# Kernel tuning notes

Hardware: AMD Instinct MI355X
Metric: run time of the kernel (lower is better)

Reference implementation:

```python
import jax, jax.numpy as jnp
import numpy as np

B, D, N = 2, 128, 100000  # batch, cubic grid edge, active voxels


def _conv(x, w):
    # valid 3D conv, NDHWC activations, DHWIO weights
    return jax.lax.conv_general_dilated(
        x, w, window_strides=(1, 1, 1), padding='VALID',
        dimension_numbers=('NDHWC', 'DHWIO', 'NDHWC'))


def setup_inputs() -> dict:
    key = jax.random.key(0)
    k = jax.random.split(key, 7)
    bidx = jax.random.randint(k[0], (N, 1), 0, B, dtype=jnp.int32)
    sp = jax.random.randint(k[1], (N, 3), 0, D, dtype=jnp.int32)
    coords = jnp.concatenate([bidx, sp], axis=1)          # [N,4] (b,z,y,x)
    voxels = jax.random.normal(k[2], (N, 3), jnp.float32)  # [N,3]
    W1 = jax.random.normal(k[3], (2, 2, 2, 3, 9), jnp.float32) * 0.2   # spconv1
    W2 = jax.random.normal(k[4], (3, 3, 3, 9, 5), jnp.float32) * 0.1   # spconv2
    W3 = jax.random.normal(k[5], (3, 3, 3, 5, 3), jnp.float32) * 0.1   # normal_conv3d
    b3 = jax.random.normal(k[6], (3,), jnp.float32) * 0.1
    return {'coords': coords, 'voxels': voxels, 'W1': W1, 'W2': W2, 'W3': W3, 'b3': b3}


def reference(coords, voxels, W1, W2, W3, b3):
    # scatter sparse voxels into a dense grid [B,D,D,D,3]
    dense = jnp.zeros((B, D, D, D, voxels.shape[-1]), voxels.dtype)
    dense = dense.at[coords[:, 0], coords[:, 1], coords[:, 2], coords[:, 3]].add(voxels)
    # SparseConv3d (stride=1, pad=0) == valid dense conv on the densified tensor
    x = _conv(dense, W1)      # [B,127,127,127,9]
    x = _conv(x, W2)          # [B,125,125,125,5]  (== ScatterDense of sparse out)
    x = _conv(x, W3) + b3     # [B,123,123,123,3]
    return jax.nn.relu(x)
```

## Files before the change

### kernel.cpp

```cpp
#include <hip/hip_runtime.h>
#include <hip/hip_bf16.h>

#define DGRID 128
#define E1 127
#define E2 125
#define E3 123

typedef __attribute__((ext_vector_type(8))) short short8;
typedef __attribute__((ext_vector_type(4))) float f32x4;
typedef __attribute__((ext_vector_type(4))) unsigned int u32x4;

static __device__ __forceinline__ unsigned short f2bf(float f) {
    union { __hip_bfloat16 h; unsigned short u; } cv;
    cv.h = __float2bfloat16(f);
    return cv.u;
}

static __device__ __forceinline__ int r3off(int row, int x) {
    return row * 384 + ((x * 16) ^ ((row & 7) << 4));
}

__global__ __launch_bounds__(256) void zero_k(float4* __restrict__ p, int n4) {
    int i = blockIdx.x * 256 + threadIdx.x;
    if (i < n4) p[i] = make_float4(0.f, 0.f, 0.f, 0.f);
}

__global__ __launch_bounds__(256) void scatter_k(const int* __restrict__ coords,
                                                 const float* __restrict__ voxels,
                                                 float* __restrict__ dense, int N) {
    int i = blockIdx.x * blockDim.x + threadIdx.x;
    if (i >= N * 3) return;
    int n = i / 3, c = i - n * 3;
    int b = coords[n * 4 + 0];
    int z = coords[n * 4 + 1];
    int y = coords[n * 4 + 2];
    int x = coords[n * 4 + 3];
    int idx = (((b * DGRID + z) * DGRID + y) * DGRID + x) * 4 + c;
    atomicAdd(&dense[idx], voxels[n * 3 + c]);
}

__global__ __launch_bounds__(256) void wcomp_k(const float* __restrict__ W1f,
                                               const float* __restrict__ W2f,
                                               float* __restrict__ W12) {
    for (int e = threadIdx.x; e < 960; e += 256) {
        const int tap = e / 15, r = e % 15;
        const int ci = r / 5, co = r % 5;
        const int KZ = tap >> 4, KY = (tap >> 2) & 3, KX = tap & 3;
        float acc = 0.f;
#pragma unroll
        for (int k1z = 0; k1z < 2; ++k1z) {
            const int k2z = KZ - k1z;
            if (k2z < 0 || k2z > 2) continue;
#pragma unroll
            for (int k1y = 0; k1y < 2; ++k1y) {
                const int k2y = KY - k1y;
                if (k2y < 0 || k2y > 2) continue;
#pragma unroll
                for (int k1x = 0; k1x < 2; ++k1x) {
                    const int k2x = KX - k1x;
                    if (k2x < 0 || k2x > 2) continue;
                    const float* w1 = W1f + ((k1z * 2 + k1y) * 2 + k1x) * 27 + ci * 9;
                    const float* w2 = W2f + ((k2z * 3 + k2y) * 3 + k2x) * 45 + co;
#pragma unroll
                    for (int m = 0; m < 9; ++m) acc += w1[m] * w2[m * 5];
                }
            }
        }
        W12[tap * 15 + r] = acc;
    }
}

__global__ __launch_bounds__(256, 4) void conv12_k(const float* __restrict__ dense,
                                                   const float* __restrict__ W12,
                                                   short* __restrict__ x2s) {
    __shared__ __align__(16) char sDD[19360];

    const int tid = threadIdx.x;
    int blk = blockIdx.x;
    const int xt  = blk & 7;  blk >>= 3;
    const int tyt = blk & 15; blk >>= 4;
    const int tzt = blk & 15; blk >>= 4;
    const int b   = blk;
    const int z0 = tzt * 8, y0 = tyt * 8, x0 = xt * 16;

    const int lane = tid & 63;
    const int col  = lane & 15;
    const int q4   = lane >> 4;
    const int wv   = tid >> 6;

    short8 B12[8];
#pragma unroll
    for (int t = 0; t < 8; ++t) {
#pragma unroll
        for (int j = 0; j < 8; ++j) {
            const int tap = 8 * t + 2 * q4 + (j >> 2);
            const int ci  = j & 3;
            float v = (ci < 3 && col < 5) ? W12[tap * 15 + ci * 5 + col] : 0.f;
            B12[t][j] = (short)f2bf(v);
        }
    }

    int offt[8];
#pragma unroll
    for (int t = 0; t < 8; ++t) {
        const int T0 = 8 * t + 2 * q4;
        const int kz = T0 >> 4, ky = (T0 >> 2) & 3, kx0 = T0 & 3;
        offt[t] = (kz * 11 + ky) * 160 + kx0 * 8;
    }

#pragma unroll 1
    for (int p = tid; p < 2299; p += 256) {
        const int xp = p % 19; int t2 = p / 19;
        const int yp = t2 % 11; const int zp = t2 / 11;
        const int gz = min(z0 + zp, DGRID - 1);
        const int gy = min(y0 + yp, DGRID - 1);
        const int gx = min(x0 + xp, DGRID - 1);
        const float4 v = *(const float4*)(dense +
            (size_t)(((b * DGRID + gz) * DGRID + gy) * DGRID + gx) * 4);
        const unsigned lo = (unsigned)f2bf(v.x) | ((unsigned)f2bf(v.y) << 16);
        const unsigned hi = (unsigned)f2bf(v.z) | ((unsigned)f2bf(v.w) << 16);
        *(uint2*)(sDD + (zp * 11 + yp) * 160 + xp * 8) = make_uint2(lo, hi);
    }
    __syncthreads();

#pragma unroll 1
    for (int gi = 0; gi < 16; ++gi) {
        const int g = wv * 16 + gi;
        const int zp = g >> 3, yp = g & 7;
        const int oz = z0 + zp, oy = y0 + yp;
        if (oz >= E2 || oy >= E2) continue;
        const int baseg = (zp * 11 + yp) * 160 + col * 8;
        f32x4 acc = {0.f, 0.f, 0.f, 0.f};
#pragma unroll
        for (int t = 0; t < 8; ++t) {
            const char* p = sDD + baseg + offt[t];
            const uint2 ra = *(const uint2*)(p);
            const uint2 rb = *(const uint2*)(p + 8);
            union { u32x4 u; short8 s; } av;
            av.u[0] = ra.x; av.u[1] = ra.y; av.u[2] = rb.x; av.u[3] = rb.y;
            acc = __builtin_amdgcn_mfma_f32_16x16x32_bf16(av.s, B12[t], acc, 0, 0, 0);
        }
        if (col < 8) {
#pragma unroll
            for (int jj = 0; jj < 4; ++jj) {
                const int ox = x0 + q4 * 4 + jj;
                if (ox < E2)
                    x2s[(size_t)(((b * E2 + oz) * E2 + oy) * E2 + ox) * 8 + col] =
                        (short)f2bf(acc[jj]);
            }
        }
    }
}

__global__ __launch_bounds__(256, 4) void conv3_k(const short* __restrict__ x2s,
                                                  const float* __restrict__ W3f,
                                                  const float* __restrict__ b3f,
                                                  float* __restrict__ out) {
    __shared__ __align__(16) char sX2[38400];

    const int tid = threadIdx.x;
    int blk = blockIdx.x;
    const int xt  = blk & 7;  blk >>= 3;
    const int tyt = blk & 15; blk >>= 4;
    const int tzt = blk & 15; blk >>= 4;
    const int b   = blk;
    const int z0 = tzt * 8, y0 = tyt * 8, x0 = xt * 16;

#pragma unroll 1
    for (int p = tid; p < 1800; p += 256) {
        const int xp = p % 18; int t2 = p / 18;
        const int yp = t2 % 10; const int zp = t2 / 10;
        const int iz = min(z0 + zp, E2 - 1);
        const int iy = min(y0 + yp, E2 - 1);
        const int ix = min(x0 + xp, E2 - 1);
        const short8 rec = *(const short8*)(x2s + (size_t)(((b * E2 + iz) * E2 + iy) * E2 + ix) * 8);
        *(short8*)(sX2 + r3off(zp * 10 + yp, xp)) = rec;
    }

    const int lane = tid & 63;
    const int col  = lane & 15;
    const int q4   = lane >> 4;
    short8 B3[7];
#pragma unroll
    for (int t = 0; t < 7; ++t) {
        const int tap = 4 * t + q4;
#pragma unroll
        for (int j = 0; j < 8; ++j) {
            float v = 0.f;
            if (tap < 27 && j < 5 && col < 3) v = W3f[(tap * 5 + j) * 3 + col];
            B3[t][j] = (short)f2bf(v);
        }
    }
    const float bias = (col < 3) ? b3f[col] : 0.f;
    __syncthreads();

    const int wv = tid >> 6;
#pragma unroll 1
    for (int gi = 0; gi < 16; ++gi) {
        const int g = wv * 16 + gi;
        const int zp = g >> 3, yp = g & 7;
        const int oz = z0 + zp, oy = y0 + yp;
        if (oz >= E3 || oy >= E3) continue;
        f32x4 acc = {0.f, 0.f, 0.f, 0.f};
#pragma unroll
        for (int t = 0; t < 7; ++t) {
            const int tap = (4 * t + q4 > 26) ? 26 : 4 * t + q4;
            const int kz = tap / 9, ky = (tap / 3) % 3, kx = tap % 3;
            const int row = (zp + kz) * 10 + (yp + ky);
            const int xi = (lane & 15) + kx;
            const short8 a = *(const short8*)(sX2 + r3off(row, xi));
            acc = __builtin_amdgcn_mfma_f32_16x16x32_bf16(a, B3[t], acc, 0, 0, 0);
        }
        if (col < 3) {
#pragma unroll
            for (int jj = 0; jj < 4; ++jj) {
                const int ox = x0 + q4 * 4 + jj;
                if (ox < E3)
                    out[(size_t)(((b * E3 + oz) * E3 + oy) * E3 + ox) * 3 + col] =
                        fmaxf(acc[jj] + bias, 0.f);
            }
        }
    }
}

extern "C" void kernel_launch(void* const* d_in, const int* in_sizes, int n_in,
                              void* d_out, int out_size, void* d_ws, size_t ws_size,
                              hipStream_t stream) {
    const int*   coords = (const int*)d_in[0];
    const float* voxels = (const float*)d_in[1];
    const float* W1     = (const float*)d_in[2];
    const float* W2     = (const float*)d_in[3];
    const float* W3     = (const float*)d_in[4];
    const float* b3     = (const float*)d_in[5];
    float* out = (float*)d_out;

    const int N = in_sizes[0] / 4;

    char* ws = (char*)d_ws;
    const size_t dense_elems = (size_t)2 * DGRID * DGRID * DGRID * 4;
    const size_t dense_bytes = dense_elems * sizeof(float);
    const size_t x2_bytes    = (size_t)2 * E2 * E2 * E2 * 8 * sizeof(short);
    float* dense = (float*)ws;
    short* x2s   = (short*)(ws + dense_bytes);
    float* W12   = (float*)(ws + dense_bytes + x2_bytes);

    const int n4 = (int)(dense_elems / 4);
    zero_k<<<(n4 + 255) / 256, 256, 0, stream>>>((float4*)dense, n4);

    scatter_k<<<(N * 3 + 255) / 256, 256, 0, stream>>>(coords, voxels, dense, N);

    wcomp_k<<<1, 256, 0, stream>>>(W1, W2, W12);

    const int nblk12 = 2 * 16 * 16 * 8;
    conv12_k<<<nblk12, 256, 0, stream>>>(dense, W12, x2s);

    const int nblk3 = 2 * 16 * 16 * 8;
    conv3_k<<<nblk3, 256, 0, stream>>>(x2s, W3, b3, out);
}
```

Baseline: 229.8 us.

## Batch rows per wave and duplicate odd-shifted LDS tile for aligned 16B loads

In conv12_k, the dense tile is stored twice in LDS, a second copy shifted by one voxel, so each MFMA A-operand becomes a single aligned 16-byte load instead of two 8-byte loads. Both conv kernels now process several output rows per wave with independent accumulators. This exposes more MFMA ILP and removes per-row index math. conv3_k drops the XOR swizzle for a padded 336-byte row stride. The costs are doubled LDS in conv12 (possibly lower occupancy), more registers, and possible bank conflicts from the changed layout.

```diff
diff --git a/kernel.cpp b/kernel.cpp
--- a/kernel.cpp
+++ b/kernel.cpp
@@ -8,16 +8,11 @@
 
 typedef __attribute__((ext_vector_type(8))) short short8;
 typedef __attribute__((ext_vector_type(4))) float f32x4;
-typedef __attribute__((ext_vector_type(4))) unsigned int u32x4;
 
 static __device__ __forceinline__ unsigned short f2bf(float f) {
     union { __hip_bfloat16 h; unsigned short u; } cv;
     cv.h = __float2bfloat16(f);
     return cv.u;
-}
-
-static __device__ __forceinline__ int r3off(int row, int x) {
-    return row * 384 + ((x * 16) ^ ((row & 7) << 4));
 }
 
 __global__ __launch_bounds__(256) void zero_k(float4* __restrict__ p, int n4) {
@@ -73,7 +68,7 @@
 __global__ __launch_bounds__(256, 4) void conv12_k(const float* __restrict__ dense,
                                                    const float* __restrict__ W12,
                                                    short* __restrict__ x2s) {
-    __shared__ __align__(16) char sDD[19360];
+    __shared__ __align__(16) char sDD[38720];
 
     const int tid = threadIdx.x;
     int blk = blockIdx.x;
@@ -100,12 +95,13 @@
         }
     }
 
-    int offt[8];
+    int ofs[8];
 #pragma unroll
     for (int t = 0; t < 8; ++t) {
         const int T0 = 8 * t + 2 * q4;
         const int kz = T0 >> 4, ky = (T0 >> 2) & 3, kx0 = T0 & 3;
-        offt[t] = (kz * 11 + ky) * 160 + kx0 * 8;
+        const int s = col + kx0;
+        ofs[t] = (kz * 11 + ky) * 160 + ((s & 1) ? (19360 + (s - 1) * 8) : (s * 8));
     }
 
 #pragma unroll 1
@@ -119,34 +115,39 @@
             (size_t)(((b * DGRID + gz) * DGRID + gy) * DGRID + gx) * 4);
         const unsigned lo = (unsigned)f2bf(v.x) | ((unsigned)f2bf(v.y) << 16);
         const unsigned hi = (unsigned)f2bf(v.z) | ((unsigned)f2bf(v.w) << 16);
-        *(uint2*)(sDD + (zp * 11 + yp) * 160 + xp * 8) = make_uint2(lo, hi);
+        const int off = (zp * 11 + yp) * 160 + xp * 8;
+        *(uint2*)(sDD + off) = make_uint2(lo, hi);
+        if (xp > 0) *(uint2*)(sDD + 19360 + off - 8) = make_uint2(lo, hi);
     }
     __syncthreads();
 
 #pragma unroll 1
-    for (int gi = 0; gi < 16; ++gi) {
-        const int g = wv * 16 + gi;
-        const int zp = g >> 3, yp = g & 7;
-        const int oz = z0 + zp, oy = y0 + yp;
-        if (oz >= E2 || oy >= E2) continue;
-        const int baseg = (zp * 11 + yp) * 160 + col * 8;
-        f32x4 acc = {0.f, 0.f, 0.f, 0.f};
+    for (int batch = 0; batch < 4; ++batch) {
+        const int zp = wv * 2 + (batch >> 1);
+        const int yb = (batch & 1) * 4;
+        const int rowb = (zp * 11 + yb) * 160;
+        f32x4 acc[4];
+#pragma unroll
+        for (int i = 0; i < 4; ++i) acc[i] = (f32x4){0.f, 0.f, 0.f, 0.f};
 #pragma unroll
         for (int t = 0; t < 8; ++t) {
-            const char* p = sDD + baseg + offt[t];
-            const uint2 ra = *(const uint2*)(p);
-            const uint2 rb = *(const uint2*)(p + 8);
-            union { u32x4 u; short8 s; } av;
-            av.u[0] = ra.x; av.u[1] = ra.y; av.u[2] = rb.x; av.u[3] = rb.y;
-            acc = __builtin_amdgcn_mfma_f32_16x16x32_bf16(av.s, B12[t], acc, 0, 0, 0);
-        }
-        if (col < 8) {
-#pragma unroll
-            for (int jj = 0; jj < 4; ++jj) {
-                const int ox = x0 + q4 * 4 + jj;
-                if (ox < E2)
-                    x2s[(size_t)(((b * E2 + oz) * E2 + oy) * E2 + ox) * 8 + col] =
-                        (short)f2bf(acc[jj]);
+            const char* pa = sDD + rowb + ofs[t];
+#pragma unroll
+            for (int i = 0; i < 4; ++i) {
+                const short8 a = *(const short8*)(pa + i * 160);
+                acc[i] = __builtin_amdgcn_mfma_f32_16x16x32_bf16(a, B12[t], acc[i], 0, 0, 0);
+            }
+        }
+        const int oz = z0 + zp;
+#pragma unroll
+        for (int i = 0; i < 4; ++i) {
+            const int oy = y0 + yb + i;
+            if (oz < E2 && oy < E2 && col < 8) {
+                short* op = x2s + (size_t)(((b * E2 + oz) * E2 + oy) * E2 + x0) * 8 +
+                            q4 * 32 + col;
+#pragma unroll
+                for (int jj = 0; jj < 4; ++jj)
+                    if (x0 + q4 * 4 + jj < E2) op[jj * 8] = (short)f2bf(acc[i][jj]);
             }
         }
     }
@@ -156,7 +157,7 @@
                                                   const float* __restrict__ W3f,
                                                   const float* __restrict__ b3f,
                                                   float* __restrict__ out) {
-    __shared__ __align__(16) char sX2[38400];
+    __shared__ __align__(16) char sX2[33600];
 
     const int tid = threadIdx.x;
     int blk = blockIdx.x;
@@ -174,13 +175,14 @@
         const int iy = min(y0 + yp, E2 - 1);
         const int ix = min(x0 + xp, E2 - 1);
         const short8 rec = *(const short8*)(x2s + (size_t)(((b * E2 + iz) * E2 + iy) * E2 + ix) * 8);
-        *(short8*)(sX2 + r3off(zp * 10 + yp, xp)) = rec;
+        *(short8*)(sX2 + (zp * 10 + yp) * 336 + xp * 16) = rec;
     }
 
     const int lane = tid & 63;
     const int col  = lane & 15;
     const int q4   = lane >> 4;
     short8 B3[7];
+    int tdelta[7];
 #pragma unroll
     for (int t = 0; t < 7; ++t) {
         const int tap = 4 * t + q4;
@@ -190,34 +192,40 @@
             if (tap < 27 && j < 5 && col < 3) v = W3f[(tap * 5 + j) * 3 + col];
             B3[t][j] = (short)f2bf(v);
         }
+        const int tc = (tap > 26) ? 26 : tap;
+        const int kz = tc / 9, ky = (tc / 3) % 3, kx = tc % 3;
+        tdelta[t] = (kz * 10 + ky) * 336 + kx * 16;
     }
     const float bias = (col < 3) ? b3f[col] : 0.f;
     __syncthreads();
 
     const int wv = tid >> 6;
 #pragma unroll 1
-    for (int gi = 0; gi < 16; ++gi) {
-        const int g = wv * 16 + gi;
-        const int zp = g >> 3, yp = g & 7;
-        const int oz = z0 + zp, oy = y0 + yp;
-        if (oz >= E3 || oy >= E3) continue;
-        f32x4 acc = {0.f, 0.f, 0.f, 0.f};
+    for (int batch = 0; batch < 2; ++batch) {
+        const int zp = wv * 2 + batch;
+        const int rowb = (zp * 10) * 336 + col * 16;
+        f32x4 acc[8];
+#pragma unroll
+        for (int i = 0; i < 8; ++i) acc[i] = (f32x4){0.f, 0.f, 0.f, 0.f};
 #pragma unroll
         for (int t = 0; t < 7; ++t) {
-            const int tap = (4 * t + q4 > 26) ? 26 : 4 * t + q4;
-            const int kz = tap / 9, ky = (tap / 3) % 3, kx = tap % 3;
-            const int row = (zp + kz) * 10 + (yp + ky);
-            const int xi = (lane & 15) + kx;
-            const short8 a = *(const short8*)(sX2 + r3off(row, xi));
-            acc = __builtin_amdgcn_mfma_f32_16x16x32_bf16(a, B3[t], acc, 0, 0, 0);
-        }
-        if (col < 3) {
-#pragma unroll
-            for (int jj = 0; jj < 4; ++jj) {
-                const int ox = x0 + q4 * 4 + jj;
-                if (ox < E3)
-                    out[(size_t)(((b * E3 + oz) * E3 + oy) * E3 + ox) * 3 + col] =
-                        fmaxf(acc[jj] + bias, 0.f);
+            const char* pa = sX2 + rowb + tdelta[t];
+#pragma unroll
+            for (int i = 0; i < 8; ++i) {
+                const short8 a = *(const short8*)(pa + i * 336);
+                acc[i] = __builtin_amdgcn_mfma_f32_16x16x32_bf16(a, B3[t], acc[i], 0, 0, 0);
+            }
+        }
+        const int oz = z0 + zp;
+#pragma unroll
+        for (int i = 0; i < 8; ++i) {
+            const int oy = y0 + i;
+            if (oz < E3 && oy < E3 && col < 3) {
+                float* op = out + (size_t)(((b * E3 + oz) * E3 + oy) * E3 + x0) * 3 +
+                            q4 * 12 + col;
+#pragma unroll
+                for (int jj = 0; jj < 4; ++jj)
+                    if (x0 + q4 * 4 + jj < E3) op[jj * 3] = fmaxf(acc[i][jj] + bias, 0.f);
             }
         }
     }
```

Result: no change. 232.3 us (+1.1%).
